# Kernel optimization log

Measured on AMD Instinct MI355X. Metric: run time of the kernel, lower is better.

Reference implementation:

```python
import jax, jax.numpy as jnp
import numpy as np

B, E_DIM, N_EXP, EXP_SZ, N_TASKS, TOPK = 16384, 512, 16, 512, 2, 3
D_IN = 2 * E_DIM      # 1024
D_HID = 4 * E_DIM     # 2048
EPS = 1e-5


def _ln(x, g, b):
    mu = jnp.mean(x, axis=-1, keepdims=True)
    var = jnp.var(x, axis=-1, keepdims=True)
    return (x - mu) * jax.lax.rsqrt(var + EPS) * g + b


def setup_inputs() -> dict:
    key = jax.random.key(0)
    ks = jax.random.split(key, 24)
    def w(k, shape, fan_in):
        return jax.random.normal(k, shape, jnp.float32) * (1.0 / np.sqrt(fan_in))
    return {
        "emb_paper": jax.random.normal(ks[0], (B, E_DIM), jnp.float32),
        "emb_reviewer": jax.random.normal(ks[1], (B, E_DIM), jnp.float32),
        # interaction encoder
        "enc_W1": w(ks[2], (D_IN, D_HID), D_IN), "enc_b1": jnp.zeros((D_HID,), jnp.float32),
        "ln1_g": jnp.ones((D_HID,), jnp.float32), "ln1_b": jnp.zeros((D_HID,), jnp.float32),
        "enc_W2": w(ks[3], (D_HID, D_IN), D_HID), "enc_b2": jnp.zeros((D_IN,), jnp.float32),
        "ln2_g": jnp.ones((D_IN,), jnp.float32), "ln2_b": jnp.zeros((D_IN,), jnp.float32),
        # per-task gates (stacked over task axis)
        "gW1": w(ks[4], (N_TASKS, D_IN, 128), D_IN), "gb1": jnp.zeros((N_TASKS, 128), jnp.float32),
        "gW2": w(ks[5], (N_TASKS, 128, N_EXP), 128), "gb2": jnp.zeros((N_TASKS, N_EXP), jnp.float32),
        # stacked experts
        "We1": w(ks[6], (N_EXP, D_IN, EXP_SZ), D_IN), "be1": jnp.zeros((N_EXP, EXP_SZ), jnp.float32),
        "We2": w(ks[7], (N_EXP, EXP_SZ, EXP_SZ), EXP_SZ), "be2": jnp.zeros((N_EXP, EXP_SZ), jnp.float32),
        # per-task towers
        "tW1": w(ks[8], (N_TASKS, EXP_SZ, 256), EXP_SZ), "tb1": jnp.zeros((N_TASKS, 256), jnp.float32),
        "tW2": w(ks[9], (N_TASKS, 256, 128), 256), "tb2": jnp.zeros((N_TASKS, 128), jnp.float32),
        "tW3": w(ks[10], (N_TASKS, 128, 1), 128), "tb3": jnp.zeros((N_TASKS, 1), jnp.float32),
        "task_idx": 0,
    }


def reference(emb_paper, emb_reviewer, enc_W1, enc_b1, ln1_g, ln1_b, enc_W2, enc_b2,
              ln2_g, ln2_b, gW1, gb1, gW2, gb2, We1, be1, We2, be2,
              tW1, tb1, tW2, tb2, tW3, tb3, task_idx):
    # interaction encoder (eval mode: dropout is identity)
    x = jnp.concatenate([emb_paper, emb_reviewer], axis=-1)          # [B, 2E]
    h = jax.nn.relu(_ln(x @ enc_W1 + enc_b1, ln1_g, ln1_b))          # [B, 4E]
    feat = _ln(h @ enc_W2 + enc_b2, ln2_g, ln2_b)                    # [B, 2E]

    # task gate -> top-k sparse softmax gates (no router noise in eval)
    g = jax.nn.relu(feat @ gW1[task_idx] + gb1[task_idx])
    logits = g @ gW2[task_idx] + gb2[task_idx]                       # [B, E]
    top_s, top_i = jax.lax.top_k(logits, TOPK)                       # [B, k]
    gates = jnp.zeros_like(logits).at[jnp.arange(logits.shape[0])[:, None], top_i].set(
        jax.nn.softmax(top_s, axis=-1))

    # dense expert stack (faithful to original: all experts computed)
    e1 = jax.nn.relu(jnp.einsum('bi,eio->beo', feat, We1) + be1[None])   # [B, E, S]
    eo = jnp.einsum('beo,eoh->beh', e1, We2) + be2[None]                 # [B, E, S]
    mix = jnp.einsum('be,beh->bh', gates, eo)                            # [B, S]

    # task tower
    t = jax.nn.relu(mix @ tW1[task_idx] + tb1[task_idx])
    t = jax.nn.relu(t @ tW2[task_idx] + tb2[task_idx])
    out = jax.nn.sigmoid(t @ tW3[task_idx] + tb3[task_idx]).squeeze(-1)  # [B]
    return out, task_idx, gates
```

## Files before the change

### kernel.cpp

```cpp
#include <hip/hip_runtime.h>

typedef __attribute__((ext_vector_type(8))) _Float16 f16x8;
typedef __attribute__((ext_vector_type(4))) float f32x4;

#define DEVINL __device__ __forceinline__

constexpr int BATCH = 16384;
constexpr int DIN   = 1024;
constexpr int DHID  = 2048;
constexpr int NEXP  = 16;
constexpr int EXPSZ = 512;
constexpr int NPAIR = BATCH * 3;

DEVINL unsigned short f2h(float v) {
  _Float16 h = (_Float16)v;
  return __builtin_bit_cast(unsigned short, h);
}
DEVINL float h2f(unsigned short u) {
  return (float)__builtin_bit_cast(_Float16, u);
}

DEVINL void gl2lds(const unsigned short* src, char* ldst) {
  __builtin_amdgcn_global_load_lds((const __attribute__((address_space(1))) void*)src,
                                   (__attribute__((address_space(3))) void*)ldst, 16, 0, 0);
}

template<int SPLIT, int ASTAGE, int AMODE, int EPI, int BK, int NYT, int TASK>
__global__ __launch_bounds__(256, SPLIT ? 2 : 3)
void mgemm_k(const unsigned short* __restrict__ A0p,
             const unsigned short* __restrict__ A1p,
             const float* __restrict__ Af0, const float* __restrict__ Af1,
             const unsigned short* __restrict__ B0p,
             const unsigned short* __restrict__ B1p,
             const float* __restrict__ biasb,
             float* __restrict__ Cf, unsigned short* __restrict__ Cb0,
             unsigned short* __restrict__ Cb1,
             const int* __restrict__ pairRow, const float* __restrict__ pairW,
             const int* __restrict__ counts, const int* __restrict__ offs,
             const int* __restrict__ taskPtr,
             int M, int N, int K)
{
  constexpr int KG = BK / 8;
  constexpr int UNITS = 128 * KG;
  constexpr int ISS = UNITS / 256;
  constexpr int NKK = BK / 32;
  constexpr int NARR = SPLIT ? 4 : 2;
  constexpr size_t BUFSZ = (size_t)NARR * UNITS * 16;
  constexpr bool EXPERT = (AMODE == 1 || AMODE == 2);
  __shared__ char smem[2 * NARR * UNITS * 16];

  int Mloc = M, rowBase = 0;
  const unsigned short* b0 = B0p;
  const unsigned short* b1 = B1p;
  const float* bias = biasb;
  if (EXPERT) {
    const int e = blockIdx.z;
    Mloc = counts[e];
    rowBase = offs[e];
    const size_t eo = (size_t)e * (size_t)K * N;
    b0 = B0p + eo;
    if (SPLIT) b1 = B1p + eo;
    bias = biasb + (size_t)e * N;
  }
  if (TASK) bias = biasb + (size_t)(*taskPtr) * N;

  const int xcd = (int)blockIdx.x & 7;
  const int j   = (int)blockIdx.x >> 3;
  const int tile0 = (xcd + 8 * (j / NYT)) * 128;
  const int col0  = (j % NYT) * 128;
  if (tile0 >= Mloc) return;

  const int tid = threadIdx.x;
  const int lane = tid & 63;
  const int wr = ((tid >> 6) >> 1) * 64;
  const int wc = ((tid >> 6) & 1) * 64;
  const int l15 = lane & 15;
  const int lg = lane >> 4;

  const int srow = tid & 127;
  size_t aoff = 0;
  const float* aF = nullptr;
  const float* aP = nullptr;
  const float* aR = nullptr;
  if (ASTAGE) {
    if (AMODE == 3) {
      aP = Af0 + (size_t)(tile0 + srow) * 512;
      aR = Af1 + (size_t)(tile0 + srow) * 512;
    } else {
      aF = Af0 + (size_t)(tile0 + srow) * K;
    }
  } else if (AMODE == 0) {
    aoff = (size_t)(tile0 + srow) * K;
  } else if (AMODE == 1) {
    int p = rowBase + tile0 + srow; p = p < NPAIR - 1 ? p : NPAIR - 1;
    aoff = (size_t)pairRow[p] * K;
  } else {
    int p = rowBase + tile0 + srow; p = p < NPAIR - 1 ? p : NPAIR - 1;
    aoff = (size_t)p * K;
  }
  const size_t boff = (size_t)(col0 + srow) * K;

  f32x4 acc[4][4];
  f32x4 acc2[4][4];
  #pragma unroll
  for (int m = 0; m < 4; ++m)
    #pragma unroll
    for (int n = 0; n < 4; ++n) {
      acc[m][n] = f32x4{0.f, 0.f, 0.f, 0.f};
      if (SPLIT) acc2[m][n] = f32x4{0.f, 0.f, 0.f, 0.f};
    }

  {
    char* dA0 = smem;
    char* dA1 = smem + UNITS * 16;
    char* dB0 = smem + (SPLIT ? 2 : 1) * UNITS * 16;
    char* dB1 = smem + 3 * (size_t)UNITS * 16;
    if (ASTAGE) {
      #pragma unroll
      for (int it = 0; it < ISS; ++it) {
        const int u = it * 256 + tid;
        const int ko = (u >> 7) * 8;
        const float* s;
        if (AMODE == 3) s = (ko < 512) ? (aP + ko) : (aR + (ko - 512));
        else            s = aF + ko;
        const float4 x0 = *(const float4*)s;
        const float4 x1 = *(const float4*)(s + 4);
        const float vv[8] = {x0.x, x0.y, x0.z, x0.w, x1.x, x1.y, x1.z, x1.w};
        f16x8 q0, q1;
        #pragma unroll
        for (int jq = 0; jq < 8; ++jq) {
          const _Float16 c0 = (_Float16)vv[jq];
          q0[jq] = c0;
          if (SPLIT) q1[jq] = (_Float16)((vv[jq] - (float)c0) * 2048.f);
        }
        *(f16x8*)(dA0 + (size_t)u * 16) = q0;
        if (SPLIT) *(f16x8*)(dA1 + (size_t)u * 16) = q1;
      }
    }
    #pragma unroll
    for (int it = 0; it < ISS; ++it) {
      const int uo = (it * 256 + (tid & 192)) * 16;
      const int ko = (it * 2 + (tid >> 7)) * 8;
      if (!ASTAGE) {
        gl2lds(A0p + aoff + ko, dA0 + uo);
        if (SPLIT) gl2lds(A1p + aoff + ko, dA1 + uo);
      }
      gl2lds(b0 + boff + ko, dB0 + uo);
      if (SPLIT) gl2lds(b1 + boff + ko, dB1 + uo);
    }
  }
  __syncthreads();

  const int NT = K / BK;
  int cur = 0;
  for (int t = 0; t < NT; ++t) {
    const int nxt = cur ^ 1;
    const int ktn = (t + 1) * BK;
    const bool hav = (t + 1 < NT);
    char* nA0 = smem + (size_t)nxt * BUFSZ;
    char* nA1 = nA0 + UNITS * 16;
    char* nB0 = nA0 + (SPLIT ? 2 : 1) * UNITS * 16;
    char* nB1 = nA0 + 3 * (size_t)UNITS * 16;

    float4 pf0[ISS], pf1[ISS];
    if (hav) {
      if (ASTAGE) {
        #pragma unroll
        for (int it = 0; it < ISS; ++it) {
          const int u = it * 256 + tid;
          const int ko = ktn + (u >> 7) * 8;
          const float* s;
          if (AMODE == 3) s = (ko < 512) ? (aP + ko) : (aR + (ko - 512));
          else            s = aF + ko;
          pf0[it] = *(const float4*)s;
          pf1[it] = *(const float4*)(s + 4);
        }
      } else {
        #pragma unroll
        for (int it = 0; it < ISS; ++it) {
          const int uo = (it * 256 + (tid & 192)) * 16;
          const int ko = ktn + (it * 2 + (tid >> 7)) * 8;
          gl2lds(A0p + aoff + ko, nA0 + uo);
          if (SPLIT) gl2lds(A1p + aoff + ko, nA1 + uo);
        }
      }
      #pragma unroll
      for (int it = 0; it < ISS; ++it) {
        const int uo = (it * 256 + (tid & 192)) * 16;
        const int ko = ktn + (it * 2 + (tid >> 7)) * 8;
        gl2lds(b0 + boff + ko, nB0 + uo);
        if (SPLIT) gl2lds(b1 + boff + ko, nB1 + uo);
      }
    }

    {
      char* cA0 = smem + (size_t)cur * BUFSZ;
      char* cA1 = cA0 + UNITS * 16;
      char* cB0 = cA0 + (SPLIT ? 2 : 1) * UNITS * 16;
      char* cB1 = cA0 + 3 * (size_t)UNITS * 16;
      __builtin_amdgcn_s_setprio(1);
      #pragma unroll
      for (int kk = 0; kk < NKK; ++kk) {
        const int g = kk * 4 + lg;
        f16x8 b0f[4], b1f[4];
        #pragma unroll
        for (int n = 0; n < 4; ++n) {
          const size_t off = (size_t)(g * 128 + wc + n * 16 + l15) * 16;
          b0f[n] = *(const f16x8*)(cB0 + off);
          if (SPLIT) b1f[n] = *(const f16x8*)(cB1 + off);
        }
        #pragma unroll
        for (int m = 0; m < 4; ++m) {
          const size_t ao = (size_t)(g * 128 + wr + m * 16 + l15) * 16;
          const f16x8 a0 = *(const f16x8*)(cA0 + ao);
          f16x8 a1;
          if (SPLIT) a1 = *(const f16x8*)(cA1 + ao);
          #pragma unroll
          for (int n = 0; n < 4; ++n) {
            if (SPLIT) {
              acc2[m][n] = __builtin_amdgcn_mfma_f32_16x16x32_f16(a1, b0f[n], acc2[m][n], 0, 0, 0);
              acc2[m][n] = __builtin_amdgcn_mfma_f32_16x16x32_f16(a0, b1f[n], acc2[m][n], 0, 0, 0);
            }
            acc[m][n] = __builtin_amdgcn_mfma_f32_16x16x32_f16(a0, b0f[n], acc[m][n], 0, 0, 0);
          }
        }
      }
      __builtin_amdgcn_s_setprio(0);
    }

    if (hav && ASTAGE) {
      #pragma unroll
      for (int it = 0; it < ISS; ++it) {
        const int u = it * 256 + tid;
        const float vv[8] = {pf0[it].x, pf0[it].y, pf0[it].z, pf0[it].w,
                             pf1[it].x, pf1[it].y, pf1[it].z, pf1[it].w};
        f16x8 q0, q1;
        #pragma unroll
        for (int jq = 0; jq < 8; ++jq) {
          const _Float16 c0 = (_Float16)vv[jq];
          q0[jq] = c0;
          if (SPLIT) q1[jq] = (_Float16)((vv[jq] - (float)c0) * 2048.f);
        }
        *(f16x8*)(nA0 + (size_t)u * 16) = q0;
        if (SPLIT) *(f16x8*)(nA1 + (size_t)u * 16) = q1;
      }
    }
    __syncthreads();
    cur = nxt;
  }

  #pragma unroll
  for (int n = 0; n < 4; ++n) {
    const int cn = col0 + wc + n * 16 + l15;
    const float bv = bias[cn];
    #pragma unroll
    for (int m = 0; m < 4; ++m) {
      const int r0 = wr + m * 16 + ((lane >> 4) << 2);
      #pragma unroll
      for (int jj = 0; jj < 4; ++jj) {
        const int rm = tile0 + r0 + jj;
        if (EXPERT && rm >= Mloc) continue;
        float v = acc[m][n][jj];
        if (SPLIT) v += acc2[m][n][jj] * (1.f / 2048.f);
        v += bv;
        const size_t ci = (size_t)(EXPERT ? (rowBase + rm) : rm) * N + cn;
        if (EPI == 0) {
          const unsigned short h0 = f2h(v);
          Cb0[ci] = h0;
          Cb1[ci] = f2h((v - h2f(h0)) * 2048.f);
        } else if (EPI == 1) {
          Cb0[ci] = f2h(fmaxf(v, 0.f));
        } else if (EPI == 2) {
          Cb0[ci] = f2h(v * pairW[rowBase + rm]);
        } else if (EPI == 3) {
          Cf[ci] = v;
        } else {
          Cf[ci] = fmaxf(v, 0.f);
        }
      }
    }
  }
}

template<int LEV, int TASK>
__global__ __launch_bounds__(256)
void transp_k(const float* __restrict__ src, unsigned short* __restrict__ d0,
              unsigned short* __restrict__ d1, const int* __restrict__ taskPtr,
              int R, int C)
{
  __shared__ float tle[32][33];
  size_t bb = (size_t)blockIdx.z * R * C;
  if (TASK) bb = (size_t)(*taskPtr) * R * C;
  const int r0 = blockIdx.x * 32, c0 = blockIdx.y * 32;
  const int x = threadIdx.x & 31, y = threadIdx.x >> 5;
  #pragma unroll
  for (int i = 0; i < 32; i += 8)
    tle[y + i][x] = src[bb + (size_t)(r0 + y + i) * C + (c0 + x)];
  __syncthreads();
  const size_t db = TASK ? 0 : (size_t)blockIdx.z * R * C;
  #pragma unroll
  for (int i = 0; i < 32; i += 8) {
    const float v = tle[x][y + i];
    const size_t di = db + (size_t)(c0 + y + i) * R + (r0 + x);
    const unsigned short h0 = f2h(v);
    d0[di] = h0;
    if (LEV > 1) d1[di] = f2h((v - h2f(h0)) * 2048.f);
  }
}

template<int COLS, bool RELU>
__global__ __launch_bounds__(256)
void ln_k(float* __restrict__ x, const float* __restrict__ g, const float* __restrict__ b)
{
  constexpr int PER = COLS / 256;
  const size_t row = blockIdx.x;
  float* xr = x + row * COLS;
  float v[PER];
  float s = 0.f, s2 = 0.f;
  #pragma unroll
  for (int i = 0; i < PER; ++i) {
    v[i] = xr[threadIdx.x + i * 256];
    s += v[i];
    s2 += v[i] * v[i];
  }
  #pragma unroll
  for (int o = 1; o < 64; o <<= 1) { s += __shfl_xor(s, o); s2 += __shfl_xor(s2, o); }
  __shared__ float ss[4], ss2[4];
  const int w = threadIdx.x >> 6;
  if ((threadIdx.x & 63) == 0) { ss[w] = s; ss2[w] = s2; }
  __syncthreads();
  s  = ss[0] + ss[1] + ss[2] + ss[3];
  s2 = ss2[0] + ss2[1] + ss2[2] + ss2[3];
  const float mu = s * (1.f / COLS);
  const float var = s2 * (1.f / COLS) - mu * mu;
  const float rs = rsqrtf(var + 1e-5f);
  #pragma unroll
  for (int i = 0; i < PER; ++i) {
    const int c = threadIdx.x + i * 256;
    float y = (v[i] - mu) * rs * g[c] + b[c];
    if (RELU) y = fmaxf(y, 0.f);
    xr[c] = y;
  }
}

template<int COLS, bool RELU>
__global__ __launch_bounds__(256)
void ln_pair_k(unsigned short* __restrict__ h0, unsigned short* __restrict__ h1,
               const float* __restrict__ g, const float* __restrict__ b)
{
  constexpr int PER = COLS / 256;
  const size_t row = blockIdx.x;
  unsigned short* r0 = h0 + row * COLS;
  unsigned short* r1 = h1 + row * COLS;
  const int c0 = threadIdx.x * PER;
  float v[PER];
  float s = 0.f, s2 = 0.f;
  #pragma unroll
  for (int i = 0; i < PER; i += 4) {
    const ushort4 a = *(const ushort4*)(r0 + c0 + i);
    const ushort4 c = *(const ushort4*)(r1 + c0 + i);
    v[i+0] = h2f(a.x) + h2f(c.x) * (1.f/2048.f);
    v[i+1] = h2f(a.y) + h2f(c.y) * (1.f/2048.f);
    v[i+2] = h2f(a.z) + h2f(c.z) * (1.f/2048.f);
    v[i+3] = h2f(a.w) + h2f(c.w) * (1.f/2048.f);
  }
  #pragma unroll
  for (int i = 0; i < PER; ++i) { s += v[i]; s2 += v[i] * v[i]; }
  #pragma unroll
  for (int o = 1; o < 64; o <<= 1) { s += __shfl_xor(s, o); s2 += __shfl_xor(s2, o); }
  __shared__ float ss[4], ss2[4];
  const int w = threadIdx.x >> 6;
  if ((threadIdx.x & 63) == 0) { ss[w] = s; ss2[w] = s2; }
  __syncthreads();
  s  = ss[0] + ss[1] + ss[2] + ss[3];
  s2 = ss2[0] + ss2[1] + ss2[2] + ss2[3];
  const float mu = s * (1.f / COLS);
  const float var = s2 * (1.f / COLS) - mu * mu;
  const float rs = rsqrtf(var + 1e-5f);
  #pragma unroll
  for (int i = 0; i < PER; i += 4) {
    ushort4 a4, c4v;
    unsigned short* ap = (unsigned short*)&a4;
    unsigned short* cp = (unsigned short*)&c4v;
    #pragma unroll
    for (int jq = 0; jq < 4; ++jq) {
      const int c = c0 + i + jq;
      float y = (v[i+jq] - mu) * rs * g[c] + b[c];
      if (RELU) y = fmaxf(y, 0.f);
      const unsigned short hh = f2h(y);
      ap[jq] = hh;
      cp[jq] = f2h((y - h2f(hh)) * 2048.f);
    }
    *(ushort4*)(r0 + c0 + i) = a4;
    *(ushort4*)(r1 + c0 + i) = c4v;
  }
}

__global__ __launch_bounds__(256)
void gate_topk_k(const float* __restrict__ g, const float* __restrict__ gW2,
                 const float* __restrict__ gb2, const int* __restrict__ taskPtr,
                 float* __restrict__ gatesOut, int* __restrict__ topkIdx,
                 float* __restrict__ topkW)
{
  const int t = *taskPtr;
  const float* W = gW2 + (size_t)t * 128 * 16;
  const float* bias = gb2 + (size_t)t * 16;
  const int lane = threadIdx.x & 63;
  const int row = blockIdx.x * 4 + (threadIdx.x >> 6);
  const float* gr = g + (size_t)row * 128;
  const int e = lane & 15;
  const int q = lane >> 4;
  float s = 0.f;
  for (int j = q * 32; j < q * 32 + 32; ++j) s = fmaf(gr[j], W[j * 16 + e], s);
  s += __shfl_xor(s, 16);
  s += __shfl_xor(s, 32);
  s += bias[e];
  float logits[16];
  #pragma unroll
  for (int i = 0; i < 16; ++i) logits[i] = __shfl(s, i);
  int i0 = 0; float v0 = logits[0];
  #pragma unroll
  for (int i = 1; i < 16; ++i) if (logits[i] > v0) { v0 = logits[i]; i0 = i; }
  int i1 = -1; float v1 = -3.4e38f;
  #pragma unroll
  for (int i = 0; i < 16; ++i) if (i != i0 && logits[i] > v1) { v1 = logits[i]; i1 = i; }
  int i2 = -1; float v2 = -3.4e38f;
  #pragma unroll
  for (int i = 0; i < 16; ++i) if (i != i0 && i != i1 && logits[i] > v2) { v2 = logits[i]; i2 = i; }
  const float ex1 = expf(v1 - v0);
  const float ex2 = expf(v2 - v0);
  const float inv = 1.f / (1.f + ex1 + ex2);
  const float p0 = inv, p1 = ex1 * inv, p2 = ex2 * inv;
  if (lane < 16) {
    const float gv = (lane == i0) ? p0 : (lane == i1) ? p1 : (lane == i2) ? p2 : 0.f;
    gatesOut[(size_t)row * 16 + lane] = gv;
  }
  if (lane == 0) {
    topkIdx[row * 3 + 0] = i0; topkIdx[row * 3 + 1] = i1; topkIdx[row * 3 + 2] = i2;
    topkW [row * 3 + 0] = p0; topkW [row * 3 + 1] = p1; topkW [row * 3 + 2] = p2;
  }
}

__global__ __launch_bounds__(256)
void hist_k(const int* __restrict__ topkIdx, int* __restrict__ chunkCnt)
{
  __shared__ int lc[NEXP];
  if (threadIdx.x < NEXP) lc[threadIdx.x] = 0;
  __syncthreads();
  const int row = blockIdx.x * 256 + threadIdx.x;
  #pragma unroll
  for (int k = 0; k < 3; ++k) atomicAdd(&lc[topkIdx[row * 3 + k]], 1);
  __syncthreads();
  if (threadIdx.x < NEXP) chunkCnt[blockIdx.x * NEXP + threadIdx.x] = lc[threadIdx.x];
}

__global__ void scanB_k(const int* __restrict__ chunkCnt, int* __restrict__ counts,
                        int* __restrict__ offs, int* __restrict__ chunkBase)
{
  if (threadIdx.x == 0) {
    int tot[NEXP];
    for (int e = 0; e < NEXP; ++e) tot[e] = 0;
    for (int c = 0; c < 64; ++c)
      for (int e = 0; e < NEXP; ++e) tot[e] += chunkCnt[c * NEXP + e];
    int a = 0;
    for (int e = 0; e < NEXP; ++e) { offs[e] = a; counts[e] = tot[e]; a += tot[e]; }
    for (int e = 0; e < NEXP; ++e) {
      int b = offs[e];
      for (int c = 0; c < 64; ++c) { chunkBase[c * NEXP + e] = b; b += chunkCnt[c * NEXP + e]; }
    }
  }
}

__global__ __launch_bounds__(256)
void fill2_k(const int* __restrict__ topkIdx, const float* __restrict__ topkW,
             const int* __restrict__ chunkBase, int* __restrict__ pairRow,
             float* __restrict__ pairW, int* __restrict__ rowPos)
{
  __shared__ int lc[NEXP];
  if (threadIdx.x < NEXP) lc[threadIdx.x] = 0;
  __syncthreads();
  const int row = blockIdx.x * 256 + threadIdx.x;
  #pragma unroll
  for (int k = 0; k < 3; ++k) {
    const int e = topkIdx[row * 3 + k];
    const int lofs = atomicAdd(&lc[e], 1);
    const int pos = chunkBase[blockIdx.x * NEXP + e] + lofs;
    pairRow[pos] = row;
    pairW[pos] = topkW[row * 3 + k];
    rowPos[row * 3 + k] = pos;
  }
}

__global__ __launch_bounds__(256)
void mixreduce_k(const unsigned short* __restrict__ eo, const int* __restrict__ rowPos,
                 unsigned short* __restrict__ mix16)
{
  const size_t row = blockIdx.x;
  const size_t p0 = rowPos[row * 3 + 0];
  const size_t p1 = rowPos[row * 3 + 1];
  const size_t p2 = rowPos[row * 3 + 2];
  for (int c = threadIdx.x; c < EXPSZ; c += 256) {
    mix16[row * EXPSZ + c] = f2h(h2f(eo[p0 * EXPSZ + c]) + h2f(eo[p1 * EXPSZ + c])
                               + h2f(eo[p2 * EXPSZ + c]));
  }
}

__global__ __launch_bounds__(256)
void tower3_k(const unsigned short* __restrict__ t2, const float* __restrict__ tW3,
              const float* __restrict__ tb3, const int* __restrict__ taskPtr,
              float* __restrict__ out)
{
  const int t = *taskPtr;
  const float* w = tW3 + (size_t)t * 128;
  const float bias = tb3[t];
  const int lane = threadIdx.x & 63;
  const int row = blockIdx.x * 4 + (threadIdx.x >> 6);
  const unsigned short* x = t2 + (size_t)row * 128;
  float s = fmaf(h2f(x[lane]), w[lane], h2f(x[lane + 64]) * w[lane + 64]);
  #pragma unroll
  for (int o = 1; o < 64; o <<= 1) s += __shfl_xor(s, o);
  if (lane == 0) out[row] = 1.f / (1.f + expf(-(s + bias)));
  if (blockIdx.x == 0 && threadIdx.x == 0) out[BATCH] = (float)t;
}

extern "C" void kernel_launch(void* const* d_in, const int* in_sizes, int n_in,
                              void* d_out, int out_size, void* d_ws, size_t ws_size,
                              hipStream_t stream)
{
  (void)in_sizes; (void)n_in; (void)out_size; (void)ws_size;
  const float* embP  = (const float*)d_in[0];
  const float* embR  = (const float*)d_in[1];
  const float* encW1 = (const float*)d_in[2];
  const float* encB1 = (const float*)d_in[3];
  const float* ln1g  = (const float*)d_in[4];
  const float* ln1b  = (const float*)d_in[5];
  const float* encW2 = (const float*)d_in[6];
  const float* encB2 = (const float*)d_in[7];
  const float* ln2g  = (const float*)d_in[8];
  const float* ln2b  = (const float*)d_in[9];
  const float* gW1   = (const float*)d_in[10];
  const float* gb1   = (const float*)d_in[11];
  const float* gW2   = (const float*)d_in[12];
  const float* gb2   = (const float*)d_in[13];
  const float* We1   = (const float*)d_in[14];
  const float* be1   = (const float*)d_in[15];
  const float* We2   = (const float*)d_in[16];
  const float* be2   = (const float*)d_in[17];
  const float* tW1   = (const float*)d_in[18];
  const float* tb1   = (const float*)d_in[19];
  const float* tW2   = (const float*)d_in[20];
  const float* tb2   = (const float*)d_in[21];
  const float* tW3   = (const float*)d_in[22];
  const float* tb3   = (const float*)d_in[23];
  const int* taskPtr = (const int*)d_in[24];

  float* out = (float*)d_out;
  char* ws = (char*)d_ws;
  const size_t MB = 1ull << 20;

  unsigned short* feat0 = (unsigned short*)(ws);
  unsigned short* feat1 = (unsigned short*)(ws + 32 * MB);
  unsigned short* mix16 = (unsigned short*)(ws + 32 * MB);
  unsigned short* t1f16 = (unsigned short*)(ws + 48 * MB);
  unsigned short* t2f16 = (unsigned short*)(ws + 56 * MB);
  float* h = (float*)(ws + 64 * MB);
  unsigned short* We1t0 = (unsigned short*)(ws + 64 * MB);
  unsigned short* We2t0 = (unsigned short*)(ws + 80 * MB);
  unsigned short* e1b   = (unsigned short*)(ws + 88 * MB);
  unsigned short* eob   = (unsigned short*)(ws + 136 * MB);
  unsigned short* W1t0  = (unsigned short*)(ws + 192 * MB);
  unsigned short* W1t1  = (unsigned short*)(ws + 196 * MB);
  unsigned short* W2t0  = (unsigned short*)(ws + 200 * MB);
  unsigned short* W2t1  = (unsigned short*)(ws + 204 * MB);
  unsigned short* gW1t0 = (unsigned short*)(ws + 200 * MB);
  unsigned short* gW1t1 = (unsigned short*)(ws + 204 * MB);
  float* gbuf = (float*)(ws + 192 * MB);
  unsigned short* tW1t = (unsigned short*)(ws + 192 * MB);
  unsigned short* tW2t = (unsigned short*)(ws + 193 * MB);
  char* small = ws + 208 * MB;
  int*   counts    = (int*)  (small);
  int*   offs      = (int*)  (small + 1024);
  int*   chunkCnt  = (int*)  (small + 2048);
  int*   chunkBase = (int*)  (small + 2048 + 4096);
  int*   topkIdx   = (int*)  (small + 16384);
  float* topkW     = (float*)(small + 16384 + 196608);
  int*   pairRow   = (int*)  (small + 16384 + 2 * 196608);
  float* pairW     = (float*)(small + 16384 + 3 * 196608);
  int*   rowPos    = (int*)  (small + 16384 + 4 * 196608);

  const dim3 blk(256, 1, 1);

  transp_k<2,0><<<dim3(DIN/32, DHID/32, 1), blk, 0, stream>>>(encW1, W1t0, W1t1, nullptr, DIN, DHID);
  mgemm_k<1,1,3,3,32,DHID/128,0><<<dim3((BATCH/128)*(DHID/128), 1, 1), blk, 0, stream>>>(
      nullptr, nullptr, embP, embR, W1t0, W1t1, encB1, h, nullptr, nullptr,
      nullptr, nullptr, nullptr, nullptr, nullptr, BATCH, DHID, DIN);
  ln_k<DHID, true><<<dim3(BATCH, 1, 1), blk, 0, stream>>>(h, ln1g, ln1b);

  transp_k<2,0><<<dim3(DHID/32, DIN/32, 1), blk, 0, stream>>>(encW2, W2t0, W2t1, nullptr, DHID, DIN);
  mgemm_k<1,1,0,0,32,DIN/128,0><<<dim3((BATCH/128)*(DIN/128), 1, 1), blk, 0, stream>>>(
      nullptr, nullptr, h, nullptr, W2t0, W2t1, encB2, nullptr, feat0, feat1,
      nullptr, nullptr, nullptr, nullptr, nullptr, BATCH, DIN, DHID);
  ln_pair_k<DIN, false><<<dim3(BATCH, 1, 1), blk, 0, stream>>>(feat0, feat1, ln2g, ln2b);

  transp_k<2,1><<<dim3(DIN/32, 128/32, 1), blk, 0, stream>>>(gW1, gW1t0, gW1t1, taskPtr, DIN, 128);
  mgemm_k<1,0,0,4,32,1,1><<<dim3(BATCH/128, 1, 1), blk, 0, stream>>>(
      feat0, feat1, nullptr, nullptr, gW1t0, gW1t1, gb1, gbuf, nullptr, nullptr,
      nullptr, nullptr, nullptr, nullptr, taskPtr, BATCH, 128, DIN);
  gate_topk_k<<<dim3(BATCH/4, 1, 1), blk, 0, stream>>>(
      gbuf, gW2, gb2, taskPtr, out + BATCH + 1, topkIdx, topkW);
  hist_k<<<dim3(BATCH/256, 1, 1), blk, 0, stream>>>(topkIdx, chunkCnt);
  scanB_k<<<dim3(1, 1, 1), dim3(64, 1, 1), 0, stream>>>(chunkCnt, counts, offs, chunkBase);
  fill2_k<<<dim3(BATCH/256, 1, 1), blk, 0, stream>>>(topkIdx, topkW, chunkBase,
                                                     pairRow, pairW, rowPos);

  transp_k<1,0><<<dim3(DIN/32, EXPSZ/32, NEXP), blk, 0, stream>>>(We1, We1t0, nullptr, nullptr, DIN, EXPSZ);
  transp_k<1,0><<<dim3(EXPSZ/32, EXPSZ/32, NEXP), blk, 0, stream>>>(We2, We2t0, nullptr, nullptr, EXPSZ, EXPSZ);

  mgemm_k<0,0,1,1,32,EXPSZ/128,0><<<dim3((BATCH/128)*(EXPSZ/128), 1, NEXP), blk, 0, stream>>>(
      feat0, nullptr, nullptr, nullptr, We1t0, nullptr, be1, nullptr, e1b, nullptr,
      pairRow, nullptr, counts, offs, nullptr, NPAIR, EXPSZ, DIN);
  mgemm_k<0,0,2,2,32,EXPSZ/128,0><<<dim3((BATCH/128)*(EXPSZ/128), 1, NEXP), blk, 0, stream>>>(
      e1b, nullptr, nullptr, nullptr, We2t0, nullptr, be2, nullptr, eob, nullptr,
      nullptr, pairW, counts, offs, nullptr, NPAIR, EXPSZ, EXPSZ);
  mixreduce_k<<<dim3(BATCH, 1, 1), blk, 0, stream>>>(eob, rowPos, mix16);

  transp_k<1,1><<<dim3(EXPSZ/32, 256/32, 1), blk, 0, stream>>>(tW1, tW1t, nullptr, taskPtr, EXPSZ, 256);
  transp_k<1,1><<<dim3(256/32, 128/32, 1), blk, 0, stream>>>(tW2, tW2t, nullptr, taskPtr, 256, 128);
  mgemm_k<0,0,0,1,32,2,1><<<dim3((BATCH/128)*2, 1, 1), blk, 0, stream>>>(
      mix16, nullptr, nullptr, nullptr, tW1t, nullptr, tb1, nullptr, t1f16, nullptr,
      nullptr, nullptr, nullptr, nullptr, taskPtr, BATCH, 256, EXPSZ);
  mgemm_k<0,0,0,1,32,1,1><<<dim3(BATCH/128, 1, 1), blk, 0, stream>>>(
      t1f16, nullptr, nullptr, nullptr, tW2t, nullptr, tb2, nullptr, t2f16, nullptr,
      nullptr, nullptr, nullptr, nullptr, taskPtr, BATCH, 128, 256);
  tower3_k<<<dim3(BATCH/4, 1, 1), blk, 0, stream>>>(t2f16, tW3, tb3, taskPtr, out);
}
```

Measured before the change: 1.057 ms.

## Triple-buffer B tiles with two-stage-ahead prefetch and explicit vmcnt waits

The shared-memory layout is split so A tiles stay double-buffered while B (weight) tiles get a three-slot ring. B is now prefetched two K-steps ahead. The plain __syncthreads is replaced by an s_waitcnt vmcnt(BOPS) that lets the newest B loads stay in flight across the barrier, which is meant to hide more global-load latency. The cost is one extra B buffer of LDS per block, which could lower occupancy. The hand-counted vmcnt depends on in-order completion of the issued loads.

```diff
diff --git a/kernel.cpp b/kernel.cpp
--- a/kernel.cpp
+++ b/kernel.cpp
@@ -44,10 +44,13 @@
   constexpr int UNITS = 128 * KG;
   constexpr int ISS = UNITS / 256;
   constexpr int NKK = BK / 32;
-  constexpr int NARR = SPLIT ? 4 : 2;
-  constexpr size_t BUFSZ = (size_t)NARR * UNITS * 16;
+  constexpr int NLV = SPLIT ? 2 : 1;
+  constexpr int LVLSZ = UNITS * 16;
+  constexpr int ABUF = NLV * LVLSZ;
+  constexpr int BBUF = NLV * LVLSZ;
+  constexpr int BOPS = NLV * ISS;
   constexpr bool EXPERT = (AMODE == 1 || AMODE == 2);
-  __shared__ char smem[2 * NARR * UNITS * 16];
+  __shared__ char smem[2 * ABUF + 3 * BBUF];
 
   int Mloc = M, rowBase = 0;
   const unsigned short* b0 = B0p;
@@ -110,11 +113,11 @@
       if (SPLIT) acc2[m][n] = f32x4{0.f, 0.f, 0.f, 0.f};
     }
 
+  const int NT = K / BK;
+
   {
     char* dA0 = smem;
-    char* dA1 = smem + UNITS * 16;
-    char* dB0 = smem + (SPLIT ? 2 : 1) * UNITS * 16;
-    char* dB1 = smem + 3 * (size_t)UNITS * 16;
+    char* dA1 = dA0 + LVLSZ;
     if (ASTAGE) {
       #pragma unroll
       for (int it = 0; it < ISS; ++it) {
@@ -136,39 +139,57 @@
         *(f16x8*)(dA0 + (size_t)u * 16) = q0;
         if (SPLIT) *(f16x8*)(dA1 + (size_t)u * 16) = q1;
       }
-    }
-    #pragma unroll
-    for (int it = 0; it < ISS; ++it) {
-      const int uo = (it * 256 + (tid & 192)) * 16;
-      const int ko = (it * 2 + (tid >> 7)) * 8;
-      if (!ASTAGE) {
+    } else {
+      #pragma unroll
+      for (int it = 0; it < ISS; ++it) {
+        const int uo = (it * 256 + (tid & 192)) * 16;
+        const int ko = (it * 2 + (tid >> 7)) * 8;
         gl2lds(A0p + aoff + ko, dA0 + uo);
         if (SPLIT) gl2lds(A1p + aoff + ko, dA1 + uo);
       }
-      gl2lds(b0 + boff + ko, dB0 + uo);
-      if (SPLIT) gl2lds(b1 + boff + ko, dB1 + uo);
-    }
-  }
-  __syncthreads();
-
-  const int NT = K / BK;
-  int cur = 0;
+    }
+    {
+      char* dB0 = smem + 2 * ABUF;
+      char* dB1 = dB0 + LVLSZ;
+      #pragma unroll
+      for (int it = 0; it < ISS; ++it) {
+        const int uo = (it * 256 + (tid & 192)) * 16;
+        const int ko = (it * 2 + (tid >> 7)) * 8;
+        gl2lds(b0 + boff + ko, dB0 + uo);
+        if (SPLIT) gl2lds(b1 + boff + ko, dB1 + uo);
+      }
+    }
+    if (NT > 1) {
+      char* dB0 = smem + 2 * ABUF + BBUF;
+      char* dB1 = dB0 + LVLSZ;
+      #pragma unroll
+      for (int it = 0; it < ISS; ++it) {
+        const int uo = (it * 256 + (tid & 192)) * 16;
+        const int ko = BK + (it * 2 + (tid >> 7)) * 8;
+        gl2lds(b0 + boff + ko, dB0 + uo);
+        if (SPLIT) gl2lds(b1 + boff + ko, dB1 + uo);
+      }
+      asm volatile("s_waitcnt vmcnt(%0) lgkmcnt(0)" :: "n"(BOPS) : "memory");
+    } else {
+      asm volatile("s_waitcnt vmcnt(0) lgkmcnt(0)" ::: "memory");
+    }
+    __builtin_amdgcn_sched_barrier(0);
+    __builtin_amdgcn_s_barrier();
+  }
+
   for (int t = 0; t < NT; ++t) {
-    const int nxt = cur ^ 1;
-    const int ktn = (t + 1) * BK;
-    const bool hav = (t + 1 < NT);
-    char* nA0 = smem + (size_t)nxt * BUFSZ;
-    char* nA1 = nA0 + UNITS * 16;
-    char* nB0 = nA0 + (SPLIT ? 2 : 1) * UNITS * 16;
-    char* nB1 = nA0 + 3 * (size_t)UNITS * 16;
+    const bool havA = (t + 1 < NT);
+    const bool havB = (t + 2 < NT);
+    char* nA0 = smem + (size_t)((t + 1) & 1) * ABUF;
+    char* nA1 = nA0 + LVLSZ;
 
     float4 pf0[ISS], pf1[ISS];
-    if (hav) {
+    if (havA) {
       if (ASTAGE) {
         #pragma unroll
         for (int it = 0; it < ISS; ++it) {
           const int u = it * 256 + tid;
-          const int ko = ktn + (u >> 7) * 8;
+          const int ko = (t + 1) * BK + (u >> 7) * 8;
           const float* s;
           if (AMODE == 3) s = (ko < 512) ? (aP + ko) : (aR + (ko - 512));
           else            s = aF + ko;
@@ -179,25 +200,29 @@
         #pragma unroll
         for (int it = 0; it < ISS; ++it) {
           const int uo = (it * 256 + (tid & 192)) * 16;
-          const int ko = ktn + (it * 2 + (tid >> 7)) * 8;
+          const int ko = (t + 1) * BK + (it * 2 + (tid >> 7)) * 8;
           gl2lds(A0p + aoff + ko, nA0 + uo);
           if (SPLIT) gl2lds(A1p + aoff + ko, nA1 + uo);
         }
       }
+    }
+    if (havB) {
+      char* pB0 = smem + 2 * ABUF + (size_t)((t + 2) % 3) * BBUF;
+      char* pB1 = pB0 + LVLSZ;
       #pragma unroll
       for (int it = 0; it < ISS; ++it) {
         const int uo = (it * 256 + (tid & 192)) * 16;
-        const int ko = ktn + (it * 2 + (tid >> 7)) * 8;
-        gl2lds(b0 + boff + ko, nB0 + uo);
-        if (SPLIT) gl2lds(b1 + boff + ko, nB1 + uo);
+        const int ko = (t + 2) * BK + (it * 2 + (tid >> 7)) * 8;
+        gl2lds(b0 + boff + ko, pB0 + uo);
+        if (SPLIT) gl2lds(b1 + boff + ko, pB1 + uo);
       }
     }
 
     {
-      char* cA0 = smem + (size_t)cur * BUFSZ;
-      char* cA1 = cA0 + UNITS * 16;
-      char* cB0 = cA0 + (SPLIT ? 2 : 1) * UNITS * 16;
-      char* cB1 = cA0 + 3 * (size_t)UNITS * 16;
+      char* cA0 = smem + (size_t)(t & 1) * ABUF;
+      char* cA1 = cA0 + LVLSZ;
+      char* cB0 = smem + 2 * ABUF + (size_t)(t % 3) * BBUF;
+      char* cB1 = cB0 + LVLSZ;
       __builtin_amdgcn_s_setprio(1);
       #pragma unroll
       for (int kk = 0; kk < NKK; ++kk) {
@@ -228,7 +253,7 @@
       __builtin_amdgcn_s_setprio(0);
     }
 
-    if (hav && ASTAGE) {
+    if (havA && ASTAGE) {
       #pragma unroll
       for (int it = 0; it < ISS; ++it) {
         const int u = it * 256 + tid;
@@ -245,8 +270,14 @@
         if (SPLIT) *(f16x8*)(nA1 + (size_t)u * 16) = q1;
       }
     }
-    __syncthreads();
-    cur = nxt;
+
+    if (havB) {
+      asm volatile("s_waitcnt vmcnt(%0) lgkmcnt(0)" :: "n"(BOPS) : "memory");
+    } else {
+      asm volatile("s_waitcnt vmcnt(0) lgkmcnt(0)" ::: "memory");
+    }
+    __builtin_amdgcn_sched_barrier(0);
+    __builtin_amdgcn_s_barrier();
   }
 
   #pragma unroll
```

Measured after the change: 1.055 ms. About the same (-0.2%).
